# Kernel tuning notes

Measured on AMD Instinct MI355X. Metric: run time of the kernel, lower is better.

## Reference

```python
import jax, jax.numpy as jnp
import numpy as np

# Standard 2D morphsnakes structuring elements (4 line filters), matching the
# repo-level global `filters` used by LSNet2.
_SE = np.zeros((4, 3, 3), dtype=np.float32)
_SE[0, 1, :] = 1.0           # horizontal line
_SE[1, :, 1] = 1.0           # vertical line
_SE[2] = np.eye(3, dtype=np.float32)          # main diagonal
_SE[3] = np.eye(3, dtype=np.float32)[::-1]    # anti-diagonal


def _dilate_stack(x, filts):
    # per-pixel: max over 3x3 window of (zero-padded x + filt), for every filter
    H, W = x.shape
    p = jnp.pad(x, 1)
    m = jnp.full((filts.shape[0], H, W), -jnp.inf, x.dtype)
    for k in range(3):
        for l in range(3):
            m = jnp.maximum(m, p[k:k + H, l:l + W][None] + filts[:, k, l][:, None, None])
    return m  # [F, H, W]


def _erode_stack(x, filts):
    # per-pixel: min over 3x3 window of (zero-padded x - filt) == -max(-(x - filt))
    H, W = x.shape
    p = jnp.pad(x, 1)
    m = jnp.full((filts.shape[0], H, W), jnp.inf, x.dtype)
    for k in range(3):
        for l in range(3):
            m = jnp.minimum(m, p[k:k + H, l:l + W][None] - filts[:, k, l][:, None, None])
    return m  # [F, H, W]


def _dilate_min(x, filts):
    return jnp.min(_dilate_stack(x, filts), axis=0)


def _erode_max(x, filts):
    return jnp.max(_erode_stack(x, filts), axis=0)


def setup_inputs() -> dict:
    key = jax.random.key(0)
    k1, k2 = jax.random.split(key)
    H = W = 2048
    inp = jax.random.uniform(k1, (H, W), dtype=jnp.float32)
    origin = jax.random.uniform(k2, (H, W), dtype=jnp.float32)
    filters = jnp.asarray(_SE)
    return {"input": inp, "origin": origin, "filters": filters}


def reference(input, origin, filters):
    x = input
    # SI o IS smoothing: dilate/min, erode/max, erode/max, dilate/min, dilate/min, erode/max
    x = _dilate_min(x, filters)
    x = _erode_max(x, filters)
    x = _erode_max(x, filters)
    x = _dilate_min(x, filters)
    x = _dilate_min(x, filters)
    x = _erode_max(x, filters)

    # balloon force with v = 1 and a flat ones(3,3) structuring element
    ones_f = jnp.ones((1, 3, 3), x.dtype)
    aux = _dilate_stack(x, ones_f)[0]
    threshold = jnp.percentile(x, 40.0)
    x = jnp.where(origin > threshold, aux, x)

    # Chan-Vese region means and update
    c0 = jnp.sum(origin * (1.0 - x)) / (jnp.sum(1.0 - x) + 1e-8)
    c1 = jnp.sum(origin * x) / (jnp.sum(x) + 1e-8)
    cv = (origin - c1) ** 2 - (origin - c0) ** 2
    x = jnp.where(cv < 0, 1.0, jnp.where(cv > 0, 0.0, x))
    return x
```

## Files before the change

kernel.cpp:

```cpp
#include <hip/hip_runtime.h>

#define HH 2048
#define WW 2048
#define NN (HH*WW)

static constexpr unsigned RANK0 = 1677721u;
static constexpr unsigned KEYLO = 0xB000u;
static constexpr unsigned KEYHI_ = 0xC000u;
static constexpr int NBINS = 4096;
static constexpr int NPART = 512;

#define TH 32
#define TW 128
#define LR 44
#define LCP 148

struct Scal {
  unsigned keyhiA, keyhiB, rA, rB;
  unsigned midA_, midB_, rA2, rB2;
  double thr, c0, c1;
};

static constexpr size_t OFF_CTL    = (size_t)NN * 4;
static constexpr size_t OFF_COARSE = OFF_CTL;
static constexpr size_t OFF_UNDER  = OFF_CTL + (size_t)NBINS * 4;
static constexpr size_t OFF_OVER   = OFF_UNDER + 4;
static constexpr size_t OFF_SCAL   = OFF_OVER + 4;
static constexpr size_t OFF_PART   = OFF_SCAL + 64;
static constexpr size_t OFF_MIDA   = OFF_PART + (size_t)NPART * 3 * 8;
static constexpr size_t OFF_MIDB   = OFF_MIDA + 1024;
static constexpr size_t OFF_LOWA   = OFF_MIDB + 1024;
static constexpr size_t OFF_LOWB   = OFF_LOWA + 1024;
static constexpr size_t WS_NEED    = OFF_LOWB + 1024;
static constexpr size_t CTL_BYTES  = WS_NEED - OFF_CTL;

__device__ __forceinline__ float mx3(float a, float b, float c){ return fmaxf(fmaxf(a,b),c); }
__device__ __forceinline__ float mn3(float a, float b, float c){ return fminf(fminf(a,b),c); }

__device__ __forceinline__ unsigned keyf(float x){
  unsigned b = __float_as_uint(x);
  return (b & 0x80000000u) ? ~b : (b | 0x80000000u);
}
__device__ __forceinline__ float keyinv(unsigned k){
  unsigned b = (k & 0x80000000u) ? (k ^ 0x80000000u) : ~k;
  return __uint_as_float(b);
}

__device__ __forceinline__ void loadrow(const float* __restrict__ src, int lr, int g, int lane,
                                        float4& v, float& L, float& R){
  v = *reinterpret_cast<const float4*>(&src[lr*LCP + 4*g]);
  L = __shfl_up(v.w, 1);
  R = __shfl_down(v.x, 1);
  if (lane == 0 || g == 0)   L = src[lr*LCP + (g ? 4*g - 1 : 0)];
  if (lane == 63 || g == 35) R = src[lr*LCP + ((g == 35) ? 143 : 4*g + 4)];
}

__device__ __forceinline__ void morph4(bool DIL,
    const float pr[6], const float cr[6], const float nr[6], float w[4]){
  #pragma unroll
  for (int i = 0; i < 4; i++){
    if (DIL){
      float Ah = mx3(cr[i],   cr[i+1], cr[i+2]);
      float Av = mx3(pr[i+1], cr[i+1], nr[i+1]);
      float Ad = mx3(pr[i],   cr[i+1], nr[i+2]);
      float Aa = mx3(pr[i+2], cr[i+1], nr[i]);
      float tm = mx3(pr[i], pr[i+1], pr[i+2]);
      float bm = mx3(nr[i], nr[i+1], nr[i+2]);
      float M9 = mx3(tm, Ah, bm);
      w[i] = fmaxf(M9, 1.0f + fminf(fminf(Ah,Av), fminf(Ad,Aa)));
    } else {
      float Bh = mn3(cr[i],   cr[i+1], cr[i+2]);
      float Bv = mn3(pr[i+1], cr[i+1], nr[i+1]);
      float Bd = mn3(pr[i],   cr[i+1], nr[i+2]);
      float Ba = mn3(pr[i+2], cr[i+1], nr[i]);
      float tm = mn3(pr[i], pr[i+1], pr[i+2]);
      float bm = mn3(nr[i], nr[i+1], nr[i+2]);
      float m9 = mn3(tm, Bh, bm);
      w[i] = fminf(m9, fmaxf(fmaxf(Bh,Bv), fmaxf(Bd,Ba)) - 1.0f);
    }
  }
}

__global__ __launch_bounds__(256)
void fused_morph_k(const float* __restrict__ in, float* __restrict__ out,
                   unsigned* __restrict__ gh, unsigned* __restrict__ under,
                   unsigned* __restrict__ over){
  __shared__ float lds[2][LR*LCP];
  const int tilec = blockIdx.x & 15;
  const int tiler = blockIdx.x >> 4;
  const int r0 = tiler*TH, c0 = tilec*TW;

  for (int idx = threadIdx.x; idx < LR*36; idx += 256){
    int lr = idx / 36, g = idx % 36;
    int gr = r0 - 6 + lr, gc = c0 - 8 + 4*g;
    float4 v = make_float4(0.f,0.f,0.f,0.f);
    if ((unsigned)gr < (unsigned)HH && (unsigned)gc < (unsigned)WW)
      v = *reinterpret_cast<const float4*>(in + (size_t)gr*WW + gc);
    *reinterpret_cast<float4*>(&lds[0][lr*LCP + 4*g]) = v;
  }
  __syncthreads();

  const int t = threadIdx.x;
  const int g = t % 36, s = t / 36;
  const bool active = (t < 252);
  const int lane = t & 63;
  const int gcBase = c0 - 8 + 4*g;
  const bool dilf[6] = {true,false,false,true,true,false};

  #pragma unroll 1
  for (int st = 0; st < 6; st++){
    const float* src = lds[st & 1];
    float*       dst = lds[(st & 1) ^ 1];
    if (active){
      const bool DIL = dilf[st];
      float4 vp, vc;  float pL,pR,cL,cR;
      loadrow(src, 6*s,     g, lane, vp, pL, pR);
      loadrow(src, 6*s + 1, g, lane, vc, cL, cR);
      #pragma unroll 1
      for (int k = 0; k < 6; k++){
        int lr = 6*s + 1 + k;
        float4 vn; float nL,nR;
        loadrow(src, lr + 1, g, lane, vn, nL, nR);
        float pr[6] = {pL, vp.x, vp.y, vp.z, vp.w, pR};
        float cr[6] = {cL, vc.x, vc.y, vc.z, vc.w, cR};
        float nr[6] = {nL, vn.x, vn.y, vn.z, vn.w, nR};
        float w[4];
        morph4(DIL, pr, cr, nr, w);
        int gr = r0 - 6 + lr;
        if ((unsigned)gr >= (unsigned)HH){
          w[0]=w[1]=w[2]=w[3]=0.f;
        } else {
          #pragma unroll
          for (int i = 0; i < 4; i++)
            if ((unsigned)(gcBase + i) >= (unsigned)WW) w[i] = 0.f;
        }
        *reinterpret_cast<float4*>(&dst[lr*LCP + 4*g]) = make_float4(w[0],w[1],w[2],w[3]);
        vp = vc; pL = cL; pR = cR;
        vc = vn; cL = nL; cR = nR;
      }
    }
    __syncthreads();
  }
  unsigned* lh = reinterpret_cast<unsigned*>(&lds[1][0]);
  for (int i = threadIdx.x; i < NBINS; i += 256) lh[i] = 0;
  __syncthreads();

  unsigned uc = 0, oc = 0;
  for (int idx = threadIdx.x; idx < TH*(TW/4); idx += 256){
    int row = idx >> 5, gg = idx & 31;
    float4 v = *reinterpret_cast<const float4*>(&lds[0][(row+6)*LCP + 8 + 4*gg]);
    *reinterpret_cast<float4*>(out + (size_t)(r0+row)*WW + c0 + 4*gg) = v;
    float vv[4] = {v.x, v.y, v.z, v.w};
    #pragma unroll
    for (int i = 0; i < 4; i++){
      unsigned key = keyf(vv[i]);
      unsigned hi = key >> 16;
      if (hi >= KEYLO && hi < KEYHI_) atomicAdd(&lh[hi - KEYLO], 1u);
      else if (hi < KEYLO)            uc++;
      else                            oc++;
    }
  }
  __syncthreads();
  for (int i = threadIdx.x; i < NBINS; i += 256){
    unsigned c = lh[i];
    if (c) atomicAdd(&gh[i], c);
  }
  if (uc) atomicAdd(under, uc);
  if (oc) atomicAdd(over, oc);
}

__global__ void scan_coarse_k(const unsigned* __restrict__ gh, const unsigned* __restrict__ under,
                              Scal* __restrict__ sc){
  __shared__ unsigned part[256];
  __shared__ unsigned excl[256];
  int t = threadIdx.x;
  unsigned loc = 0;
  #pragma unroll
  for (int i = 0; i < NBINS/256; i++) loc += gh[t*(NBINS/256) + i];
  part[t] = loc;
  __syncthreads();
  if (t == 0){
    unsigned run = under[0];
    for (int i = 0; i < 256; i++){ excl[i] = run; run += part[i]; }
  }
  __syncthreads();
  unsigned run = excl[t];
  const unsigned r0 = RANK0, r1 = RANK0 + 1;
  #pragma unroll
  for (int i = 0; i < NBINS/256; i++){
    unsigned idx = t*(NBINS/256) + i;
    unsigned cc = gh[idx];
    if (cc){
      if (r0 >= run && r0 - run < cc){ sc->keyhiA = KEYLO + idx; sc->rA = r0 - run; }
      if (r1 >= run && r1 - run < cc){ sc->keyhiB = KEYLO + idx; sc->rB = r1 - run; }
    }
    run += cc;
  }
}

__global__ __launch_bounds__(256)
void fine_mid_k(const float* __restrict__ x, const Scal* __restrict__ sc,
                unsigned* __restrict__ midA, unsigned* __restrict__ midB){
  __shared__ unsigned hA[256], hB[256];
  hA[threadIdx.x] = 0; hB[threadIdx.x] = 0;
  __syncthreads();
  unsigned ha = sc->keyhiA, hb = sc->keyhiB;
  bool dup = (ha == hb);
  const int nItems = NN/4;
  for (int it = blockIdx.x*blockDim.x + threadIdx.x; it < nItems; it += gridDim.x*blockDim.x){
    float4 v = reinterpret_cast<const float4*>(x)[it];
    float vv[4] = {v.x, v.y, v.z, v.w};
    #pragma unroll
    for (int t = 0; t < 4; t++){
      unsigned key = keyf(vv[t]);
      unsigned hi = key >> 16;
      if (hi == ha)      atomicAdd(&hA[(key >> 8) & 0xFFu], 1u);
      else if (hi == hb) atomicAdd(&hB[(key >> 8) & 0xFFu], 1u);
    }
  }
  __syncthreads();
  unsigned ca = hA[threadIdx.x];
  if (ca) atomicAdd(&midA[threadIdx.x], ca);
  if (!dup){
    unsigned cb = hB[threadIdx.x];
    if (cb) atomicAdd(&midB[threadIdx.x], cb);
  }
}

__global__ void scan_mid_k(const unsigned* __restrict__ midA, const unsigned* __restrict__ midB,
                           Scal* __restrict__ sc){
  __shared__ unsigned h[256], excl[256];
  int t = threadIdx.x;
  bool dup = (sc->keyhiA == sc->keyhiB);
  unsigned rA = sc->rA, rB = sc->rB;
  h[t] = midA[t];
  __syncthreads();
  if (t == 0){ unsigned run = 0; for (int i = 0; i < 256; i++){ excl[i] = run; run += h[i]; } }
  __syncthreads();
  if (rA >= excl[t] && rA - excl[t] < h[t]){ sc->midA_ = (unsigned)t; sc->rA2 = rA - excl[t]; }
  if (dup && rB >= excl[t] && rB - excl[t] < h[t]){ sc->midB_ = (unsigned)t; sc->rB2 = rB - excl[t]; }
  if (!dup){
    __syncthreads();
    h[t] = midB[t];
    __syncthreads();
    if (t == 0){ unsigned run = 0; for (int i = 0; i < 256; i++){ excl[i] = run; run += h[i]; } }
    __syncthreads();
    if (rB >= excl[t] && rB - excl[t] < h[t]){ sc->midB_ = (unsigned)t; sc->rB2 = rB - excl[t]; }
  }
}

__global__ __launch_bounds__(256)
void fine_low_k(const float* __restrict__ x, const Scal* __restrict__ sc,
                unsigned* __restrict__ lowA, unsigned* __restrict__ lowB){
  __shared__ unsigned hA[256], hB[256];
  hA[threadIdx.x] = 0; hB[threadIdx.x] = 0;
  __syncthreads();
  unsigned ha = sc->keyhiA, hb = sc->keyhiB;
  unsigned ma = sc->midA_, mb = sc->midB_;
  bool dup = (ha == hb) && (ma == mb);
  const int nItems = NN/4;
  for (int it = blockIdx.x*blockDim.x + threadIdx.x; it < nItems; it += gridDim.x*blockDim.x){
    float4 v = reinterpret_cast<const float4*>(x)[it];
    float vv[4] = {v.x, v.y, v.z, v.w};
    #pragma unroll
    for (int t = 0; t < 4; t++){
      unsigned key = keyf(vv[t]);
      unsigned hi = key >> 16;
      unsigned m  = (key >> 8) & 0xFFu;
      if (hi == ha && m == ma)      atomicAdd(&hA[key & 0xFFu], 1u);
      else if (hi == hb && m == mb) atomicAdd(&hB[key & 0xFFu], 1u);
    }
  }
  __syncthreads();
  unsigned ca = hA[threadIdx.x];
  if (ca) atomicAdd(&lowA[threadIdx.x], ca);
  if (!dup){
    unsigned cb = hB[threadIdx.x];
    if (cb) atomicAdd(&lowB[threadIdx.x], cb);
  }
}

__global__ void scan_low_k(const unsigned* __restrict__ lowA, const unsigned* __restrict__ lowB,
                           Scal* __restrict__ sc){
  __shared__ unsigned h[256], excl[256];
  __shared__ unsigned kfound[2];
  int t = threadIdx.x;
  bool dup = (sc->keyhiA == sc->keyhiB) && (sc->midA_ == sc->midB_);
  unsigned rA2 = sc->rA2, rB2 = sc->rB2;
  h[t] = lowA[t];
  __syncthreads();
  if (t == 0){ unsigned run = 0; for (int i = 0; i < 256; i++){ excl[i] = run; run += h[i]; } }
  __syncthreads();
  if (rA2 >= excl[t] && rA2 - excl[t] < h[t]) kfound[0] = (unsigned)t;
  if (dup && rB2 >= excl[t] && rB2 - excl[t] < h[t]) kfound[1] = (unsigned)t;
  if (!dup){
    __syncthreads();
    h[t] = lowB[t];
    __syncthreads();
    if (t == 0){ unsigned run = 0; for (int i = 0; i < 256; i++){ excl[i] = run; run += h[i]; } }
    __syncthreads();
    if (rB2 >= excl[t] && rB2 - excl[t] < h[t]) kfound[1] = (unsigned)t;
  }
  __syncthreads();
  if (t == 0){
    unsigned ka = (sc->keyhiA << 16) | (sc->midA_ << 8) | kfound[0];
    unsigned kb = (sc->keyhiB << 16) | (sc->midB_ << 8) | kfound[1];
    double va = (double)keyinv(ka), vb = (double)keyinv(kb);
    const double FRAC = 0.4*(double)(NN-1) - (double)RANK0;
    sc->thr = va + (vb - va) * FRAC;
  }
}

__device__ __forceinline__ void load6(const float* __restrict__ p, int row, int q, float r[6]){
  if (row < 0 || row >= HH){
    r[0]=r[1]=r[2]=r[3]=r[4]=r[5]=0.f;
    return;
  }
  const float* rp = p + (size_t)row * WW;
  float4 cc = *reinterpret_cast<const float4*>(rp + q);
  r[0] = (q > 0) ? rp[q-1] : 0.f;
  r[1]=cc.x; r[2]=cc.y; r[3]=cc.z; r[4]=cc.w;
  r[5] = (q+4 < WW) ? rp[q+4] : 0.f;
}

__global__ __launch_bounds__(256)
void balloon_k(const float* __restrict__ x, const float* __restrict__ orig,
               float* __restrict__ xb, const Scal* __restrict__ sc, double* __restrict__ part){
  double thr = sc->thr;
  double s0 = 0.0, s1 = 0.0, s2 = 0.0;
  const int nItems = NN/4;
  for (int it = blockIdx.x*blockDim.x + threadIdx.x; it < nItems; it += gridDim.x*blockDim.x){
    int i = it >> 9;
    int q = (it & 511) << 2;
    float a[6], b[6], c[6];
    load6(x, i-1, q, a);
    load6(x, i,   q, b);
    load6(x, i+1, q, c);
    float4 og = *reinterpret_cast<const float4*>(orig + (size_t)i*WW + q);
    float ov[4] = {og.x, og.y, og.z, og.w};
    float r[4];
    #pragma unroll
    for (int t = 0; t < 4; t++){
      float M9 = mx3(mx3(a[t],a[t+1],a[t+2]), mx3(b[t],b[t+1],b[t+2]), mx3(c[t],c[t+1],c[t+2]));
      float aux = 1.0f + M9;
      float nx = ((double)ov[t] > thr) ? aux : b[t+1];
      r[t] = nx;
      s0 += (double)ov[t];
      s1 += (double)nx;
      s2 += (double)ov[t] * (double)nx;
    }
    *reinterpret_cast<float4*>(xb + (size_t)i*WW + q) = make_float4(r[0],r[1],r[2],r[3]);
  }
  for (int off = 32; off > 0; off >>= 1){
    s0 += __shfl_down(s0, off);
    s1 += __shfl_down(s1, off);
    s2 += __shfl_down(s2, off);
  }
  __shared__ double red[4][3];
  int lane = threadIdx.x & 63, wv = threadIdx.x >> 6;
  if (lane == 0){ red[wv][0] = s0; red[wv][1] = s1; red[wv][2] = s2; }
  __syncthreads();
  if (threadIdx.x == 0){
    part[blockIdx.x*3+0] = red[0][0]+red[1][0]+red[2][0]+red[3][0];
    part[blockIdx.x*3+1] = red[0][1]+red[1][1]+red[2][1]+red[3][1];
    part[blockIdx.x*3+2] = red[0][2]+red[1][2]+red[2][2]+red[3][2];
  }
}

__global__ void c0c1_k(const double* __restrict__ part, Scal* __restrict__ sc){
  int t = threadIdx.x;
  double s0 = 0, s1 = 0, s2 = 0;
  for (int b = t; b < NPART; b += 256){
    s0 += part[b*3+0]; s1 += part[b*3+1]; s2 += part[b*3+2];
  }
  for (int off = 32; off > 0; off >>= 1){
    s0 += __shfl_down(s0, off);
    s1 += __shfl_down(s1, off);
    s2 += __shfl_down(s2, off);
  }
  __shared__ double red[4][3];
  int lane = t & 63, wv = t >> 6;
  if (lane == 0){ red[wv][0] = s0; red[wv][1] = s1; red[wv][2] = s2; }
  __syncthreads();
  if (t == 0){
    double So = red[0][0]+red[1][0]+red[2][0]+red[3][0];
    double Sx = red[0][1]+red[1][1]+red[2][1]+red[3][1];
    double Sox= red[0][2]+red[1][2]+red[2][2]+red[3][2];
    sc->c0 = (So - Sox) / ((double)NN - Sx + 1e-8);
    sc->c1 = Sox / (Sx + 1e-8);
  }
}

__global__ __launch_bounds__(256)
void final_k(const float* __restrict__ orig, const float* __restrict__ xb,
             const Scal* __restrict__ sc, float* __restrict__ out){
  double c0 = sc->c0, c1 = sc->c1;
  const int nItems = NN/4;
  for (int it = blockIdx.x*blockDim.x + threadIdx.x; it < nItems; it += gridDim.x*blockDim.x){
    float4 og = reinterpret_cast<const float4*>(orig)[it];
    float4 xv = reinterpret_cast<const float4*>(xb)[it];
    float ov[4] = {og.x, og.y, og.z, og.w};
    float xx[4] = {xv.x, xv.y, xv.z, xv.w};
    float r[4];
    #pragma unroll
    for (int t = 0; t < 4; t++){
      double o = (double)ov[t];
      double d1 = o - c1, d0 = o - c0;
      double cv = d1*d1 - d0*d0;
      r[t] = (cv < 0.0) ? 1.0f : ((cv > 0.0) ? 0.0f : xx[t]);
    }
    reinterpret_cast<float4*>(out)[it] = make_float4(r[0],r[1],r[2],r[3]);
  }
}

extern "C" void kernel_launch(void* const* d_in, const int* in_sizes, int n_in,
                              void* d_out, int out_size, void* d_ws, size_t ws_size,
                              hipStream_t stream) {
  const float* input  = (const float*)d_in[0];
  const float* origin = (const float*)d_in[1];
  float* out = (float*)d_out;

  char* ws = (char*)d_ws;
  float*    bufA   = (float*)ws;
  unsigned* coarse = (unsigned*)(ws + OFF_COARSE);
  unsigned* under  = (unsigned*)(ws + OFF_UNDER);
  unsigned* over   = (unsigned*)(ws + OFF_OVER);
  Scal*     scal   = (Scal*)(ws + OFF_SCAL);
  double*   part   = (double*)(ws + OFF_PART);
  unsigned* midA   = (unsigned*)(ws + OFF_MIDA);
  unsigned* midB   = (unsigned*)(ws + OFF_MIDB);
  unsigned* lowA   = (unsigned*)(ws + OFF_LOWA);
  unsigned* lowB   = (unsigned*)(ws + OFF_LOWB);

  hipMemsetAsync(ws + OFF_CTL, 0, CTL_BYTES, stream);

  fused_morph_k<<<(HH/TH)*(WW/TW), 256, 0, stream>>>(input, out, coarse, under, over);

  scan_coarse_k<<<1, 256, 0, stream>>>(coarse, under, scal);
  fine_mid_k<<<1024, 256, 0, stream>>>(out, scal, midA, midB);
  scan_mid_k<<<1, 256, 0, stream>>>(midA, midB, scal);
  fine_low_k<<<1024, 256, 0, stream>>>(out, scal, lowA, lowB);
  scan_low_k<<<1, 256, 0, stream>>>(lowA, lowB, scal);

  balloon_k<<<NPART, 256, 0, stream>>>(out, origin, bufA, scal, part);
  c0c1_k<<<1, 256, 0, stream>>>(part, scal);
  final_k<<<2048, 256, 0, stream>>>(origin, bufA, scal, out);
}
```

Before: 131.2 us.

## Single-buffer LDS morphology, pack histogram bins, and raise grid sizes

The fused morphology kernel drops its double-buffered shared tile. Each thread now keeps its six output rows in registers and writes them back in place after a barrier, which halves the tile's shared-memory footprint so more blocks can fit per CU. Neighbour columns are read directly from LDS instead of through cross-lane shuffles. The local histogram packs two 16-bit counters per word, which also shrinks shared memory. Grid sizes for the fine histogram passes and the balloon partial-sum kernel are raised, at the cost of an extra barrier per stage, higher register pressure, and more partial sums to reduce.

```diff
diff --git a/kernel.cpp b/kernel.cpp
--- a/kernel.cpp
+++ b/kernel.cpp
@@ -8,7 +8,7 @@
 static constexpr unsigned KEYLO = 0xB000u;
 static constexpr unsigned KEYHI_ = 0xC000u;
 static constexpr int NBINS = 4096;
-static constexpr int NPART = 512;
+static constexpr int NPART = 2048;
 
 #define TH 32
 #define TW 128
@@ -46,13 +46,12 @@
   return __uint_as_float(b);
 }
 
-__device__ __forceinline__ void loadrow(const float* __restrict__ src, int lr, int g, int lane,
-                                        float4& v, float& L, float& R){
-  v = *reinterpret_cast<const float4*>(&src[lr*LCP + 4*g]);
-  L = __shfl_up(v.w, 1);
-  R = __shfl_down(v.x, 1);
-  if (lane == 0 || g == 0)   L = src[lr*LCP + (g ? 4*g - 1 : 0)];
-  if (lane == 63 || g == 35) R = src[lr*LCP + ((g == 35) ? 143 : 4*g + 4)];
+__device__ __forceinline__ void loadwin(const float* __restrict__ src, int rowbase,
+                                        int colL, int colC, int colR, float w[6]){
+  float4 v = *reinterpret_cast<const float4*>(&src[rowbase + colC]);
+  w[0] = src[rowbase + colL];
+  w[1] = v.x; w[2] = v.y; w[3] = v.z; w[4] = v.w;
+  w[5] = src[rowbase + colR];
 }
 
 __device__ __forceinline__ void morph4(bool DIL,
@@ -85,7 +84,8 @@
 void fused_morph_k(const float* __restrict__ in, float* __restrict__ out,
                    unsigned* __restrict__ gh, unsigned* __restrict__ under,
                    unsigned* __restrict__ over){
-  __shared__ float lds[2][LR*LCP];
+  __shared__ float lds[LR*LCP];
+  __shared__ unsigned lh[NBINS/2];
   const int tilec = blockIdx.x & 15;
   const int tiler = blockIdx.x >> 4;
   const int r0 = tiler*TH, c0 = tilec*TW;
@@ -96,37 +96,33 @@
     float4 v = make_float4(0.f,0.f,0.f,0.f);
     if ((unsigned)gr < (unsigned)HH && (unsigned)gc < (unsigned)WW)
       v = *reinterpret_cast<const float4*>(in + (size_t)gr*WW + gc);
-    *reinterpret_cast<float4*>(&lds[0][lr*LCP + 4*g]) = v;
+    *reinterpret_cast<float4*>(&lds[lr*LCP + 4*g]) = v;
   }
   __syncthreads();
 
   const int t = threadIdx.x;
   const int g = t % 36, s = t / 36;
   const bool active = (t < 252);
-  const int lane = t & 63;
+  const int colC = 4*g;
+  const int colL = g ? 4*g - 1 : 0;
+  const int colR = (g == 35) ? 143 : 4*g + 4;
   const int gcBase = c0 - 8 + 4*g;
   const bool dilf[6] = {true,false,false,true,true,false};
 
   #pragma unroll 1
   for (int st = 0; st < 6; st++){
-    const float* src = lds[st & 1];
-    float*       dst = lds[(st & 1) ^ 1];
+    float o0[4], o1[4], o2[4], o3[4], o4[4], o5[4];
     if (active){
       const bool DIL = dilf[st];
-      float4 vp, vc;  float pL,pR,cL,cR;
-      loadrow(src, 6*s,     g, lane, vp, pL, pR);
-      loadrow(src, 6*s + 1, g, lane, vc, cL, cR);
-      #pragma unroll 1
+      float p[6], c[6], n[6];
+      loadwin(lds, (6*s)*LCP,     colL, colC, colR, p);
+      loadwin(lds, (6*s + 1)*LCP, colL, colC, colR, c);
+      #pragma unroll
       for (int k = 0; k < 6; k++){
-        int lr = 6*s + 1 + k;
-        float4 vn; float nL,nR;
-        loadrow(src, lr + 1, g, lane, vn, nL, nR);
-        float pr[6] = {pL, vp.x, vp.y, vp.z, vp.w, pR};
-        float cr[6] = {cL, vc.x, vc.y, vc.z, vc.w, cR};
-        float nr[6] = {nL, vn.x, vn.y, vn.z, vn.w, nR};
-        float w[4];
-        morph4(DIL, pr, cr, nr, w);
-        int gr = r0 - 6 + lr;
+        float* w = (k==0)?o0:(k==1)?o1:(k==2)?o2:(k==3)?o3:(k==4)?o4:o5;
+        loadwin(lds, (6*s + 2 + k)*LCP, colL, colC, colR, n);
+        morph4(DIL, p, c, n, w);
+        int gr = r0 - 6 + 6*s + 1 + k;
         if ((unsigned)gr >= (unsigned)HH){
           w[0]=w[1]=w[2]=w[3]=0.f;
         } else {
@@ -134,36 +130,50 @@
           for (int i = 0; i < 4; i++)
             if ((unsigned)(gcBase + i) >= (unsigned)WW) w[i] = 0.f;
         }
-        *reinterpret_cast<float4*>(&dst[lr*LCP + 4*g]) = make_float4(w[0],w[1],w[2],w[3]);
-        vp = vc; pL = cL; pR = cR;
-        vc = vn; cL = nL; cR = nR;
+        #pragma unroll
+        for (int i = 0; i < 6; i++){ p[i] = c[i]; c[i] = n[i]; }
       }
     }
     __syncthreads();
-  }
-  unsigned* lh = reinterpret_cast<unsigned*>(&lds[1][0]);
-  for (int i = threadIdx.x; i < NBINS; i += 256) lh[i] = 0;
+    if (active){
+      *reinterpret_cast<float4*>(&lds[(6*s+1)*LCP + colC]) = make_float4(o0[0],o0[1],o0[2],o0[3]);
+      *reinterpret_cast<float4*>(&lds[(6*s+2)*LCP + colC]) = make_float4(o1[0],o1[1],o1[2],o1[3]);
+      *reinterpret_cast<float4*>(&lds[(6*s+3)*LCP + colC]) = make_float4(o2[0],o2[1],o2[2],o2[3]);
+      *reinterpret_cast<float4*>(&lds[(6*s+4)*LCP + colC]) = make_float4(o3[0],o3[1],o3[2],o3[3]);
+      *reinterpret_cast<float4*>(&lds[(6*s+5)*LCP + colC]) = make_float4(o4[0],o4[1],o4[2],o4[3]);
+      *reinterpret_cast<float4*>(&lds[(6*s+6)*LCP + colC]) = make_float4(o5[0],o5[1],o5[2],o5[3]);
+    }
+    __syncthreads();
+  }
+
+  for (int i = threadIdx.x; i < NBINS/2; i += 256) lh[i] = 0;
   __syncthreads();
 
   unsigned uc = 0, oc = 0;
-  for (int idx = threadIdx.x; idx < TH*(TW/4); idx += 256){
+  #pragma unroll
+  for (int ii = 0; ii < 4; ii++){
+    int idx = threadIdx.x + ii*256;
     int row = idx >> 5, gg = idx & 31;
-    float4 v = *reinterpret_cast<const float4*>(&lds[0][(row+6)*LCP + 8 + 4*gg]);
+    float4 v = *reinterpret_cast<const float4*>(&lds[(row+6)*LCP + 8 + 4*gg]);
     *reinterpret_cast<float4*>(out + (size_t)(r0+row)*WW + c0 + 4*gg) = v;
     float vv[4] = {v.x, v.y, v.z, v.w};
     #pragma unroll
     for (int i = 0; i < 4; i++){
       unsigned key = keyf(vv[i]);
       unsigned hi = key >> 16;
-      if (hi >= KEYLO && hi < KEYHI_) atomicAdd(&lh[hi - KEYLO], 1u);
-      else if (hi < KEYLO)            uc++;
-      else                            oc++;
-    }
-  }
-  __syncthreads();
-  for (int i = threadIdx.x; i < NBINS; i += 256){
-    unsigned c = lh[i];
-    if (c) atomicAdd(&gh[i], c);
+      if (hi >= KEYLO && hi < KEYHI_){
+        unsigned bin = hi - KEYLO;
+        atomicAdd(&lh[bin >> 1], 1u << ((bin & 1) << 4));
+      }
+      else if (hi < KEYLO) uc++;
+      else                 oc++;
+    }
+  }
+  __syncthreads();
+  for (int i = threadIdx.x; i < NBINS/2; i += 256){
+    unsigned w = lh[i];
+    if (w & 0xFFFFu)  atomicAdd(&gh[2*i],   w & 0xFFFFu);
+    if (w >> 16)      atomicAdd(&gh[2*i+1], w >> 16);
   }
   if (uc) atomicAdd(under, uc);
   if (oc) atomicAdd(over, oc);
@@ -437,9 +447,9 @@
   fused_morph_k<<<(HH/TH)*(WW/TW), 256, 0, stream>>>(input, out, coarse, under, over);
 
   scan_coarse_k<<<1, 256, 0, stream>>>(coarse, under, scal);
-  fine_mid_k<<<1024, 256, 0, stream>>>(out, scal, midA, midB);
+  fine_mid_k<<<2048, 256, 0, stream>>>(out, scal, midA, midB);
   scan_mid_k<<<1, 256, 0, stream>>>(midA, midB, scal);
-  fine_low_k<<<1024, 256, 0, stream>>>(out, scal, lowA, lowB);
+  fine_low_k<<<2048, 256, 0, stream>>>(out, scal, lowA, lowB);
   scan_low_k<<<1, 256, 0, stream>>>(lowA, lowB, scal);
 
   balloon_k<<<NPART, 256, 0, stream>>>(out, origin, bufA, scal, part);
```

After: 147.7 us. 1.13x slower.

## Process two tiles per morph block with register prefetch and packed LDS histogram

Applied to the files above, without the earlier changes.

The fused morph kernel now runs 512 blocks, each handling two tiles. The second tile's input is prefetched into registers while the first tile is computed, which is meant to hide global load latency and halve the block count. The LDS histogram moves to a separate buffer of packed 16-bit counters, so it no longer needs its own zeroing pass in the ping-pong buffer. Balloon loads neighbouring pixels with wave shuffles instead of scalar loads, and the fine kernel and balloon grids are enlarged. The trade-offs are higher register pressure from the 7 float4 prefetch registers, fewer resident waves, and a 16-bit counter limit per bin.

```diff
diff --git a/kernel.cpp b/kernel.cpp
--- a/kernel.cpp
+++ b/kernel.cpp
@@ -8,7 +8,8 @@
 static constexpr unsigned KEYLO = 0xB000u;
 static constexpr unsigned KEYHI_ = 0xC000u;
 static constexpr int NBINS = 4096;
-static constexpr int NPART = 512;
+static constexpr int NPART = 2048;
+static constexpr int MORPH_BLOCKS = 512;
 
 #define TH 32
 #define TW 128
@@ -25,14 +26,14 @@
 static constexpr size_t OFF_COARSE = OFF_CTL;
 static constexpr size_t OFF_UNDER  = OFF_CTL + (size_t)NBINS * 4;
 static constexpr size_t OFF_OVER   = OFF_UNDER + 4;
-static constexpr size_t OFF_SCAL   = OFF_OVER + 4;
-static constexpr size_t OFF_PART   = OFF_SCAL + 64;
-static constexpr size_t OFF_MIDA   = OFF_PART + (size_t)NPART * 3 * 8;
+static constexpr size_t OFF_MIDA   = OFF_OVER + 4;
 static constexpr size_t OFF_MIDB   = OFF_MIDA + 1024;
 static constexpr size_t OFF_LOWA   = OFF_MIDB + 1024;
 static constexpr size_t OFF_LOWB   = OFF_LOWA + 1024;
-static constexpr size_t WS_NEED    = OFF_LOWB + 1024;
-static constexpr size_t CTL_BYTES  = WS_NEED - OFF_CTL;
+static constexpr size_t CTL_END    = OFF_LOWB + 1024;
+static constexpr size_t CTL_BYTES  = CTL_END - OFF_CTL;
+static constexpr size_t OFF_SCAL   = CTL_END;
+static constexpr size_t OFF_PART   = OFF_SCAL + 64;
 
 __device__ __forceinline__ float mx3(float a, float b, float c){ return fmaxf(fmaxf(a,b),c); }
 __device__ __forceinline__ float mn3(float a, float b, float c){ return fminf(fminf(a,b),c); }
@@ -86,84 +87,128 @@
                    unsigned* __restrict__ gh, unsigned* __restrict__ under,
                    unsigned* __restrict__ over){
   __shared__ float lds[2][LR*LCP];
-  const int tilec = blockIdx.x & 15;
-  const int tiler = blockIdx.x >> 4;
-  const int r0 = tiler*TH, c0 = tilec*TW;
-
-  for (int idx = threadIdx.x; idx < LR*36; idx += 256){
-    int lr = idx / 36, g = idx % 36;
-    int gr = r0 - 6 + lr, gc = c0 - 8 + 4*g;
-    float4 v = make_float4(0.f,0.f,0.f,0.f);
-    if ((unsigned)gr < (unsigned)HH && (unsigned)gc < (unsigned)WW)
-      v = *reinterpret_cast<const float4*>(in + (size_t)gr*WW + gc);
-    *reinterpret_cast<float4*>(&lds[0][lr*LCP + 4*g]) = v;
-  }
-  __syncthreads();
+  __shared__ unsigned lh[NBINS/2];
+  for (int i = threadIdx.x; i < NBINS/2; i += 256) lh[i] = 0;
 
   const int t = threadIdx.x;
   const int g = t % 36, s = t / 36;
   const bool active = (t < 252);
   const int lane = t & 63;
-  const int gcBase = c0 - 8 + 4*g;
   const bool dilf[6] = {true,false,false,true,true,false};
 
+  int tile = blockIdx.x;
+  {
+    const int r0 = (tile >> 4)*TH, c0 = (tile & 15)*TW;
+    for (int idx = t; idx < LR*36; idx += 256){
+      int lr = idx / 36, gq = idx % 36;
+      int gr = r0 - 6 + lr, gc = c0 - 8 + 4*gq;
+      float4 v = make_float4(0.f,0.f,0.f,0.f);
+      if ((unsigned)gr < (unsigned)HH && (unsigned)gc < (unsigned)WW)
+        v = *reinterpret_cast<const float4*>(in + (size_t)gr*WW + gc);
+      *reinterpret_cast<float4*>(&lds[0][lr*LCP + 4*gq]) = v;
+    }
+  }
+  __syncthreads();
+
+  unsigned uc = 0, oc = 0;
+  float4 pref[7];
+
   #pragma unroll 1
-  for (int st = 0; st < 6; st++){
-    const float* src = lds[st & 1];
-    float*       dst = lds[(st & 1) ^ 1];
-    if (active){
-      const bool DIL = dilf[st];
-      float4 vp, vc;  float pL,pR,cL,cR;
-      loadrow(src, 6*s,     g, lane, vp, pL, pR);
-      loadrow(src, 6*s + 1, g, lane, vc, cL, cR);
-      #pragma unroll 1
-      for (int k = 0; k < 6; k++){
-        int lr = 6*s + 1 + k;
-        float4 vn; float nL,nR;
-        loadrow(src, lr + 1, g, lane, vn, nL, nR);
-        float pr[6] = {pL, vp.x, vp.y, vp.z, vp.w, pR};
-        float cr[6] = {cL, vc.x, vc.y, vc.z, vc.w, cR};
-        float nr[6] = {nL, vn.x, vn.y, vn.z, vn.w, nR};
-        float w[4];
-        morph4(DIL, pr, cr, nr, w);
-        int gr = r0 - 6 + lr;
-        if ((unsigned)gr >= (unsigned)HH){
-          w[0]=w[1]=w[2]=w[3]=0.f;
-        } else {
-          #pragma unroll
-          for (int i = 0; i < 4; i++)
-            if ((unsigned)(gcBase + i) >= (unsigned)WW) w[i] = 0.f;
+  for (int tt = 0; tt < 2; tt++){
+    const int r0 = (tile >> 4)*TH, c0 = (tile & 15)*TW;
+    if (tt == 0){
+      const int tile1 = blockIdx.x + MORPH_BLOCKS;
+      const int r1 = (tile1 >> 4)*TH, c1 = (tile1 & 15)*TW;
+      #pragma unroll
+      for (int j = 0; j < 7; j++){
+        int idx = t + j*256;
+        float4 v = make_float4(0.f,0.f,0.f,0.f);
+        if (idx < LR*36){
+          int lr = idx / 36, gq = idx % 36;
+          int gr = r1 - 6 + lr, gc = c1 - 8 + 4*gq;
+          if ((unsigned)gr < (unsigned)HH && (unsigned)gc < (unsigned)WW)
+            v = *reinterpret_cast<const float4*>(in + (size_t)gr*WW + gc);
         }
-        *reinterpret_cast<float4*>(&dst[lr*LCP + 4*g]) = make_float4(w[0],w[1],w[2],w[3]);
-        vp = vc; pL = cL; pR = cR;
-        vc = vn; cL = nL; cR = nR;
+        pref[j] = v;
       }
     }
-    __syncthreads();
-  }
-  unsigned* lh = reinterpret_cast<unsigned*>(&lds[1][0]);
-  for (int i = threadIdx.x; i < NBINS; i += 256) lh[i] = 0;
-  __syncthreads();
-
-  unsigned uc = 0, oc = 0;
-  for (int idx = threadIdx.x; idx < TH*(TW/4); idx += 256){
-    int row = idx >> 5, gg = idx & 31;
-    float4 v = *reinterpret_cast<const float4*>(&lds[0][(row+6)*LCP + 8 + 4*gg]);
-    *reinterpret_cast<float4*>(out + (size_t)(r0+row)*WW + c0 + 4*gg) = v;
-    float vv[4] = {v.x, v.y, v.z, v.w};
+    const int gcBase = c0 - 8 + 4*g;
+
+    #pragma unroll 1
+    for (int st = 0; st < 6; st++){
+      const float* src = lds[st & 1];
+      float*       dst = lds[(st & 1) ^ 1];
+      if (active){
+        const bool DIL = dilf[st];
+        float4 vp, vc;  float pL,pR,cL,cR;
+        loadrow(src, 6*s,     g, lane, vp, pL, pR);
+        loadrow(src, 6*s + 1, g, lane, vc, cL, cR);
+        #pragma unroll 1
+        for (int k = 0; k < 6; k++){
+          int lr = 6*s + 1 + k;
+          float4 vn; float nL,nR;
+          loadrow(src, lr + 1, g, lane, vn, nL, nR);
+          float pr[6] = {pL, vp.x, vp.y, vp.z, vp.w, pR};
+          float cr[6] = {cL, vc.x, vc.y, vc.z, vc.w, cR};
+          float nr[6] = {nL, vn.x, vn.y, vn.z, vn.w, nR};
+          float w[4];
+          morph4(DIL, pr, cr, nr, w);
+          int gr = r0 - 6 + lr;
+          if ((unsigned)gr >= (unsigned)HH){
+            w[0]=w[1]=w[2]=w[3]=0.f;
+          } else {
+            #pragma unroll
+            for (int i = 0; i < 4; i++)
+              if ((unsigned)(gcBase + i) >= (unsigned)WW) w[i] = 0.f;
+          }
+          *reinterpret_cast<float4*>(&dst[lr*LCP + 4*g]) = make_float4(w[0],w[1],w[2],w[3]);
+          vp = vc; pL = cL; pR = cR;
+          vc = vn; cL = nL; cR = nR;
+        }
+      }
+      __syncthreads();
+    }
+
     #pragma unroll
-    for (int i = 0; i < 4; i++){
-      unsigned key = keyf(vv[i]);
-      unsigned hi = key >> 16;
-      if (hi >= KEYLO && hi < KEYHI_) atomicAdd(&lh[hi - KEYLO], 1u);
-      else if (hi < KEYLO)            uc++;
-      else                            oc++;
-    }
-  }
-  __syncthreads();
-  for (int i = threadIdx.x; i < NBINS; i += 256){
-    unsigned c = lh[i];
-    if (c) atomicAdd(&gh[i], c);
+    for (int ii = 0; ii < 4; ii++){
+      int idx = t + ii*256;
+      int row = idx >> 5, gg = idx & 31;
+      float4 v = *reinterpret_cast<const float4*>(&lds[0][(row+6)*LCP + 8 + 4*gg]);
+      *reinterpret_cast<float4*>(out + (size_t)(r0+row)*WW + c0 + 4*gg) = v;
+      float vv[4] = {v.x, v.y, v.z, v.w};
+      #pragma unroll
+      for (int i = 0; i < 4; i++){
+        unsigned key = keyf(vv[i]);
+        unsigned hi = key >> 16;
+        if (hi >= KEYLO && hi < KEYHI_){
+          unsigned bin = hi - KEYLO;
+          atomicAdd(&lh[bin >> 1], 1u << ((bin & 1) << 4));
+        }
+        else if (hi < KEYLO) uc++;
+        else                 oc++;
+      }
+    }
+
+    if (tt == 0){
+      __syncthreads();
+      #pragma unroll
+      for (int j = 0; j < 7; j++){
+        int idx = t + j*256;
+        if (idx < LR*36){
+          int lr = idx / 36, gq = idx % 36;
+          *reinterpret_cast<float4*>(&lds[0][lr*LCP + 4*gq]) = pref[j];
+        }
+      }
+      __syncthreads();
+      tile += MORPH_BLOCKS;
+    }
+  }
+
+  __syncthreads();
+  for (int i = threadIdx.x; i < NBINS/2; i += 256){
+    unsigned w = lh[i];
+    if (w & 0xFFFFu) atomicAdd(&gh[2*i],   w & 0xFFFFu);
+    if (w >> 16)     atomicAdd(&gh[2*i+1], w >> 16);
   }
   if (uc) atomicAdd(under, uc);
   if (oc) atomicAdd(over, oc);
@@ -311,16 +356,21 @@
   }
 }
 
-__device__ __forceinline__ void load6(const float* __restrict__ p, int row, int q, float r[6]){
-  if (row < 0 || row >= HH){
-    r[0]=r[1]=r[2]=r[3]=r[4]=r[5]=0.f;
+__device__ __forceinline__ void growin(const float* __restrict__ p, int row, int q, int lane,
+                                       float w[6]){
+  if ((unsigned)row >= (unsigned)HH){
+    w[0]=w[1]=w[2]=w[3]=w[4]=w[5]=0.f;
     return;
   }
   const float* rp = p + (size_t)row * WW;
-  float4 cc = *reinterpret_cast<const float4*>(rp + q);
-  r[0] = (q > 0) ? rp[q-1] : 0.f;
-  r[1]=cc.x; r[2]=cc.y; r[3]=cc.z; r[4]=cc.w;
-  r[5] = (q+4 < WW) ? rp[q+4] : 0.f;
+  float4 v = *reinterpret_cast<const float4*>(rp + 4*q);
+  float L = __shfl_up(v.w, 1);
+  float R = __shfl_down(v.x, 1);
+  if (q == 0)            L = 0.f;
+  else if (lane == 0)    L = rp[4*q - 1];
+  if (q == 511)          R = 0.f;
+  else if (lane == 63)   R = rp[4*q + 4];
+  w[0]=L; w[1]=v.x; w[2]=v.y; w[3]=v.z; w[4]=v.w; w[5]=R;
 }
 
 __global__ __launch_bounds__(256)
@@ -329,14 +379,15 @@
   double thr = sc->thr;
   double s0 = 0.0, s1 = 0.0, s2 = 0.0;
   const int nItems = NN/4;
+  const int lane = threadIdx.x & 63;
   for (int it = blockIdx.x*blockDim.x + threadIdx.x; it < nItems; it += gridDim.x*blockDim.x){
     int i = it >> 9;
-    int q = (it & 511) << 2;
+    int q = it & 511;
     float a[6], b[6], c[6];
-    load6(x, i-1, q, a);
-    load6(x, i,   q, b);
-    load6(x, i+1, q, c);
-    float4 og = *reinterpret_cast<const float4*>(orig + (size_t)i*WW + q);
+    growin(x, i-1, q, lane, a);
+    growin(x, i,   q, lane, b);
+    growin(x, i+1, q, lane, c);
+    float4 og = *reinterpret_cast<const float4*>(orig + (size_t)i*WW + 4*q);
     float ov[4] = {og.x, og.y, og.z, og.w};
     float r[4];
     #pragma unroll
@@ -349,7 +400,7 @@
       s1 += (double)nx;
       s2 += (double)ov[t] * (double)nx;
     }
-    *reinterpret_cast<float4*>(xb + (size_t)i*WW + q) = make_float4(r[0],r[1],r[2],r[3]);
+    *reinterpret_cast<float4*>(xb + (size_t)i*WW + 4*q) = make_float4(r[0],r[1],r[2],r[3]);
   }
   for (int off = 32; off > 0; off >>= 1){
     s0 += __shfl_down(s0, off);
@@ -357,7 +408,7 @@
     s2 += __shfl_down(s2, off);
   }
   __shared__ double red[4][3];
-  int lane = threadIdx.x & 63, wv = threadIdx.x >> 6;
+  int wv = threadIdx.x >> 6;
   if (lane == 0){ red[wv][0] = s0; red[wv][1] = s1; red[wv][2] = s2; }
   __syncthreads();
   if (threadIdx.x == 0){
@@ -425,21 +476,21 @@
   unsigned* coarse = (unsigned*)(ws + OFF_COARSE);
   unsigned* under  = (unsigned*)(ws + OFF_UNDER);
   unsigned* over   = (unsigned*)(ws + OFF_OVER);
-  Scal*     scal   = (Scal*)(ws + OFF_SCAL);
-  double*   part   = (double*)(ws + OFF_PART);
   unsigned* midA   = (unsigned*)(ws + OFF_MIDA);
   unsigned* midB   = (unsigned*)(ws + OFF_MIDB);
   unsigned* lowA   = (unsigned*)(ws + OFF_LOWA);
   unsigned* lowB   = (unsigned*)(ws + OFF_LOWB);
+  Scal*     scal   = (Scal*)(ws + OFF_SCAL);
+  double*   part   = (double*)(ws + OFF_PART);
 
   hipMemsetAsync(ws + OFF_CTL, 0, CTL_BYTES, stream);
 
-  fused_morph_k<<<(HH/TH)*(WW/TW), 256, 0, stream>>>(input, out, coarse, under, over);
+  fused_morph_k<<<MORPH_BLOCKS, 256, 0, stream>>>(input, out, coarse, under, over);
 
   scan_coarse_k<<<1, 256, 0, stream>>>(coarse, under, scal);
-  fine_mid_k<<<1024, 256, 0, stream>>>(out, scal, midA, midB);
+  fine_mid_k<<<2048, 256, 0, stream>>>(out, scal, midA, midB);
   scan_mid_k<<<1, 256, 0, stream>>>(midA, midB, scal);
-  fine_low_k<<<1024, 256, 0, stream>>>(out, scal, lowA, lowB);
+  fine_low_k<<<2048, 256, 0, stream>>>(out, scal, lowA, lowB);
   scan_low_k<<<1, 256, 0, stream>>>(lowA, lowB, scal);
 
   balloon_k<<<NPART, 256, 0, stream>>>(out, origin, bufA, scal, part);
```

After: 143.6 us. +9.5%, slower.
